# Kernel tuning notes

Hardware: AMD Instinct MI355X
Metric: run time of the kernel (lower is better)

Reference implementation:

```python
import jax, jax.numpy as jnp
import numpy as np

B, T, M, D, K, L = 128, 50, 4, 64, 64, 16  # batch, seq len, num_beh, embed dim, num_classes, capsule_length
NUM_ITEMS = 100000
R_ITERS = 3


def _dyn_gru(x, C, Wx, bx, Wh, bh):
    """Dynamic capsule GRU. x: [B,M,T,D], C: [B,M,T,K,L] (routing state modulates update gate).
    Returns final hidden beh_e [B,M,K,L] and per-step candidate states beh_N [B,M,T,K,L]."""
    # precompute input projections for all steps: [B,M,T,3,K,L]
    gi = (jnp.einsum('bmtd,mdg->bmtg', x, Wx) + bx[:, None, :]).reshape(x.shape[0], M, T, 3, K, L)

    def step(h, inp):
        gi_t, C_t = inp  # gi_t: [B,M,3,K,L], C_t: [B,M,K,L]
        gh = (jnp.einsum('bmkl,mklg->bmkg', h, Wh) + bh).reshape(h.shape[0], M, K, 3, L)
        r = jax.nn.sigmoid(gi_t[:, :, 0] + gh[:, :, :, 0])
        z = jax.nn.sigmoid(gi_t[:, :, 1] + gh[:, :, :, 1] + C_t)  # dynamic gate via routing state C
        n = jnp.tanh(gi_t[:, :, 2] + r * gh[:, :, :, 2])
        h_new = (1.0 - z) * n + z * h
        return h_new, n

    h0 = jnp.zeros((x.shape[0], M, K, L), x.dtype)
    h_fin, ns = jax.lax.scan(step, h0, (jnp.moveaxis(gi, 2, 0), jnp.moveaxis(C, 2, 0)))
    return h_fin, jnp.moveaxis(ns, 0, 2)


def setup_inputs() -> dict:
    key = jax.random.key(0)
    ks = jax.random.split(key, 9)
    names = ['purchase_seq', 'cart_seq', 'fav_seq', 'click_seq']
    seqs = {n: jax.random.randint(k, (B, T), 0, NUM_ITEMS + 1) for n, k in zip(names, ks[:4])}
    item_emb = jax.random.normal(ks[4], (NUM_ITEMS + 1, D), jnp.float32) * 0.02
    item_emb = item_emb.at[0].set(0.0)  # padding_idx=0
    W = 0.01 * jax.random.uniform(ks[5], (K, L, M, K), jnp.float32)
    W_coef = 0.1 * jax.random.normal(ks[6], (K, D + L, L), jnp.float32)
    alpha = jnp.ones((1,), jnp.float32) * K
    w = jnp.ones((K,), jnp.float32)
    bias = jnp.zeros((K,), jnp.float32)
    gru_Wx = 0.05 * jax.random.normal(ks[7], (M, D, 3 * K * L), jnp.float32)
    gru_bx = jnp.zeros((M, 3 * K * L), jnp.float32)
    gru_Wh = 0.05 * jax.random.normal(ks[8], (M, K, L, 3 * L), jnp.float32)
    gru_bh = jnp.zeros((M, K, 3 * L), jnp.float32)
    return dict(**seqs, item_emb=item_emb, W=W, W_coef=W_coef, alpha=alpha, w=w, bias=bias,
                gru_Wx=gru_Wx, gru_bx=gru_bx, gru_Wh=gru_Wh, gru_bh=gru_bh)


def reference(purchase_seq, cart_seq, fav_seq, click_seq, item_emb, W, W_coef,
              alpha, w, bias, gru_Wx, gru_bx, gru_Wh, gru_bh):
    sg = jax.lax.stop_gradient

    def embed(seq):
        mask = (seq != 0).astype(item_emb.dtype)[..., None]
        return item_emb[seq] * mask

    x = jnp.stack([embed(purchase_seq), embed(cart_seq), embed(fav_seq), embed(click_seq)], axis=1)  # [B,M,T,D]
    bsz = x.shape[0]
    b = jnp.zeros((bsz, K, K, 1), x.dtype)
    C = jnp.zeros((bsz, M, T, K, L), x.dtype)

    # routing iterations (all GRU outputs / W / alpha / w / bias / item_emb detached; W_coef live)
    for _ in range(R_ITERS - 1):
        beh_e, beh_N = _dyn_gru(sg(x), sg(C), sg(gru_Wx), sg(gru_bx), sg(gru_Wh), sg(gru_bh))
        beh_e = sg(beh_e).transpose(0, 2, 1, 3)  # [B,K,M,L]
        u = jnp.einsum('bctd,cdtC->bcCd', beh_e, sg(W))  # [B,K,K,L]
        c = jax.nn.softmax(b, axis=2)
        v = sg(alpha) * jnp.sum(c * u, axis=1)  # [B,K,L]
        v_ = jnp.linalg.norm(v, axis=-1) * sg(w) + sg(bias)  # [B,K]
        E = sg(item_emb)
        p = jax.nn.softmax(v_ @ E.T, axis=-1) @ E  # [B,D]
        p = jnp.broadcast_to(p[:, None, :], (bsz, K, D))
        r = jnp.einsum('bcd,cdD->bcD', jnp.concatenate([p, v], axis=-1), W_coef)  # [B,K,L]
        b = b + jnp.sum(u * r[:, None], axis=-1, keepdims=True)
        C = C + sg(beh_N) * r[:, None, None]

    beh_e, _ = _dyn_gru(x, C, gru_Wx, gru_bx, gru_Wh, gru_bh)
    beh_e = beh_e.transpose(0, 2, 1, 3)
    u_hat = jnp.einsum('bctd,cdtC->bcCd', beh_e, W)
    c = jax.nn.softmax(b, axis=2)
    v = alpha * jnp.sum(c * u_hat, axis=1)
    v_ = jnp.linalg.norm(v, axis=-1) * w + bias
    return v_ @ item_emb.T  # [B, num_items+1]
```

## Files before the change

### kernel.cpp

```cpp
#include <hip/hip_runtime.h>
#include <hip/hip_bf16.h>
#include <cstdint>
#include <cstddef>

#define B_   128
#define T_   50
#define M_   4
#define D_   64
#define K_   64
#define L_   16
#define NIT  100001
#define NBP3 256
#define CHUNK3 391
#define PSTRIDE 8320

typedef unsigned short u16;
typedef unsigned int   u32;
typedef __attribute__((ext_vector_type(8))) short short8;
typedef __attribute__((ext_vector_type(4))) short short4v;
typedef __attribute__((ext_vector_type(4))) float f32x4;

__device__ __forceinline__ float bf2f(u16 v){ u32 u = ((u32)v)<<16; float f; __builtin_memcpy(&f,&u,4); return f; }
__device__ __forceinline__ u16 f2bf(float f){
  u32 u; __builtin_memcpy(&u,&f,4);
  u32 r = (u + 0x7FFFu + ((u>>16)&1u)) >> 16;
  return (u16)r;
}
__device__ __forceinline__ float fexp(float x){ return __builtin_amdgcn_exp2f(x*1.4426950408889634f); }
__device__ __forceinline__ float fsig(float x){ return __builtin_amdgcn_rcpf(1.0f + fexp(-x)); }
__device__ __forceinline__ float ftanh(float x){ return 1.0f - 2.0f*__builtin_amdgcn_rcpf(1.0f + fexp(2.0f*x)); }
__device__ __forceinline__ void unpack8(const u32* s, short8& h, short8& l){
  #pragma unroll
  for (int q=0;q<8;q++){ h[q]=(short)(s[q]&0xFFFFu); l[q]=(short)(s[q]>>16); }
}

#define MFMA32(A,Bv,C) __builtin_amdgcn_mfma_f32_16x16x32_bf16(A,Bv,C,0,0,0)

#if __has_builtin(__builtin_amdgcn_mfma_f32_16x16x16bf16_1k)
__device__ __forceinline__ f32x4 mfma16(short4v a, short4v b, f32x4 c){
  return __builtin_amdgcn_mfma_f32_16x16x16bf16_1k(a,b,c,0,0,0);
}
#elif __has_builtin(__builtin_amdgcn_mfma_f32_16x16x16_bf16)
__device__ __forceinline__ f32x4 mfma16(short4v a, short4v b, f32x4 c){
  return __builtin_amdgcn_mfma_f32_16x16x16_bf16(a,b,c,0,0,0);
}
#else
__device__ __forceinline__ f32x4 mfma16(short4v a, short4v b, f32x4 c){
  asm("v_mfma_f32_16x16x16_bf16 %0, %1, %2, %0" : "+v"(c) : "v"(a), "v"(b));
  return c;
}
#endif

__global__ __launch_bounds__(256) void k_prep_x(const int* __restrict__ s0, const int* __restrict__ s1,
  const int* __restrict__ s2, const int* __restrict__ s3, const float* __restrict__ E,
  u16* __restrict__ xh, u16* __restrict__ xl)
{
  int id = blockIdx.x*256 + threadIdx.x;
  int e8 = id & 7;
  int rm = id >> 3;
  int m = rm / 6400; int r = rm - m*6400;
  int t = r >> 7, b = r & 127;
  const int* sq = (m==0)? s0 : (m==1)? s1 : (m==2)? s2 : s3;
  int idx = sq[b*T_ + t];
  float sc = (idx==0)? 0.0f : 1.0f;
  const float4* ep = (const float4*)(E + (size_t)idx*64 + e8*8);
  float4 v0 = ep[0], v1 = ep[1];
  float vals[8] = {v0.x,v0.y,v0.z,v0.w,v1.x,v1.y,v1.z,v1.w};
  u32 hw[4], lw[4];
  #pragma unroll
  for (int q=0;q<4;q++){
    float f0 = vals[2*q]*sc, f1 = vals[2*q+1]*sc;
    u16 h0 = f2bf(f0), h1 = f2bf(f1);
    u16 l0 = f2bf(f0 - bf2f(h0)), l1 = f2bf(f1 - bf2f(h1));
    hw[q] = (u32)h0 | ((u32)h1<<16);
    lw[q] = (u32)l0 | ((u32)l1<<16);
  }
  size_t off = (size_t)rm*64 + e8*8;
  uint4 hv; hv.x=hw[0]; hv.y=hw[1]; hv.z=hw[2]; hv.w=hw[3];
  uint4 lv; lv.x=lw[0]; lv.y=lw[1]; lv.z=lw[2]; lv.w=lw[3];
  *(uint4*)(xh + off) = hv;
  *(uint4*)(xl + off) = lv;
}

__global__ __launch_bounds__(256) void k_prep_w(const float* __restrict__ Wx,
  u16* __restrict__ wh, u16* __restrict__ wl)
{
  __shared__ float tl[64][65];
  int m = blockIdx.x / 48, gt = blockIdx.x % 48;
  for (int it=0; it<16; ++it){
    int li = threadIdx.x + it*256;
    int dl = li >> 6, gl = li & 63;
    tl[dl][gl] = Wx[((size_t)m*64 + dl)*3072 + gt*64 + gl];
  }
  __syncthreads();
  for (int it=0; it<2; ++it){
    int unit = threadIdx.x + it*256;
    int gl = unit >> 3, d8 = unit & 7;
    u32 hw[4], lw[4];
    #pragma unroll
    for (int q=0;q<4;q++){
      float f0 = tl[d8*8+2*q][gl], f1 = tl[d8*8+2*q+1][gl];
      u16 h0 = f2bf(f0), h1 = f2bf(f1);
      u16 l0 = f2bf(f0 - bf2f(h0)), l1 = f2bf(f1 - bf2f(h1));
      hw[q] = (u32)h0 | ((u32)h1<<16);
      lw[q] = (u32)l0 | ((u32)l1<<16);
    }
    size_t off = ((size_t)m*3072 + gt*64 + gl)*64 + d8*8;
    uint4 hv; hv.x=hw[0]; hv.y=hw[1]; hv.z=hw[2]; hv.w=hw[3];
    uint4 lv; lv.x=lw[0]; lv.y=lw[1]; lv.z=lw[2]; lv.w=lw[3];
    *(uint4*)(wh + off) = hv;
    *(uint4*)(wl + off) = lv;
  }
}

template<int PASS>
__global__ __launch_bounds__(256,2) void k_gru_mfma(
  const u16* __restrict__ xh, const u16* __restrict__ xl,
  const u16* __restrict__ wh, const u16* __restrict__ wl,
  const float* __restrict__ Wh, const float* __restrict__ bx, const float* __restrict__ bhp,
  const float* __restrict__ rp1, const float* __restrict__ rp2,
  const u16* __restrict__ Nr1, const u16* __restrict__ Nr2,
  u16* __restrict__ Nw, float* __restrict__ behE)
{
  int tid = threadIdx.x;
  int lane = tid & 63;
  int n16 = lane & 15, quad = lane >> 4;
  int j0 = quad*4;
  int wid = blockIdx.x*4 + (tid>>6);
  int bt = wid & 7, k = (wid>>3)&63, m = wid>>9;
  int b = bt*16 + n16;

  short8 WxH[3][2], WxL[3][2];
  #pragma unroll
  for (int g=0; g<3; ++g){
    int grow = g*1024 + k*16 + n16;
    #pragma unroll
    for (int c=0; c<2; ++c){
      size_t off = ((size_t)(m*3072 + grow))*64 + c*32 + quad*8;
      WxH[g][c] = *(const short8*)(wh + off);
      WxL[g][c] = *(const short8*)(wl + off);
    }
  }
  const float* whp = Wh + ((size_t)(m*64+k)*16)*48;
  short4v WhH[3], WhL[3];
  #pragma unroll
  for (int g=0; g<3; ++g){
    short4v hhv, llv;
    #pragma unroll
    for (int i=0;i<4;i++){
      float w = whp[(j0+i)*48 + g*16 + n16];
      u16 hbits = f2bf(w);
      hhv[i] = (short)hbits;
      llv[i] = (short)f2bf(w - bf2f(hbits));
    }
    WhH[g]=hhv; WhL[g]=llv;
  }
  float biasv[3][4], bhn[4];
  #pragma unroll
  for (int g=0; g<3; ++g)
    #pragma unroll
    for (int rg=0; rg<4; ++rg){
      int j = j0+rg;
      float tb = bx[m*3072 + g*1024 + k*16 + j];
      if (g<2) tb += bhp[(m*64+k)*48 + g*16 + j];
      biasv[g][rg] = tb;
    }
  #pragma unroll
  for (int rg=0; rg<4; ++rg) bhn[rg] = bhp[(m*64+k)*48 + 32 + j0 + rg];

  float rv1[4]={0.f,0.f,0.f,0.f}, rv2[4]={0.f,0.f,0.f,0.f};
  if (PASS>=2){
    float4 q = *(const float4*)(rp1 + ((size_t)b*64+k)*16 + j0);
    rv1[0]=q.x; rv1[1]=q.y; rv1[2]=q.z; rv1[3]=q.w;
  }
  if (PASS==3){
    float4 q = *(const float4*)(rp2 + ((size_t)b*64+k)*16 + j0);
    rv2[0]=q.x; rv2[1]=q.y; rv2[2]=q.z; rv2[3]=q.w;
  }

  size_t xrow  = ((size_t)m*6400 + bt*16 + n16)*64 + quad*8;
  size_t nbase = ((size_t)(m*64+k))*102400 + (size_t)b*16 + j0;

  short4v hH = {0,0,0,0}, hL = {0,0,0,0};
  float hprev[4] = {0.f,0.f,0.f,0.f};

  short8 cBh0 = *(const short8*)(xh + xrow);
  short8 cBh1 = *(const short8*)(xh + xrow + 32);
  short8 cBl0 = *(const short8*)(xl + xrow);
  short8 cBl1 = *(const short8*)(xl + xrow + 32);
  uint2 cN1 = {0,0}, cN2 = {0,0};
  if (PASS>=2) cN1 = *(const uint2*)(Nr1 + nbase);
  if (PASS==3) cN2 = *(const uint2*)(Nr2 + nbase);

  for (int t=0;t<50;++t){
    short8 nBh0, nBh1, nBl0, nBl1; uint2 nN1={0,0}, nN2={0,0};
    if (t<49){
      size_t xo = xrow + (size_t)(t+1)*8192;
      nBh0 = *(const short8*)(xh + xo);
      nBh1 = *(const short8*)(xh + xo + 32);
      nBl0 = *(const short8*)(xl + xo);
      nBl1 = *(const short8*)(xl + xo + 32);
      if (PASS>=2) nN1 = *(const uint2*)(Nr1 + nbase + (size_t)(t+1)*2048);
      if (PASS==3) nN2 = *(const uint2*)(Nr2 + nbase + (size_t)(t+1)*2048);
    }
    f32x4 giA[3];
    #pragma unroll
    for (int g=0; g<3; ++g){
      f32x4 a = {biasv[g][0], biasv[g][1], biasv[g][2], biasv[g][3]};
      a = MFMA32(WxH[g][0], cBh0, a);
      a = MFMA32(WxH[g][1], cBh1, a);
      a = MFMA32(WxL[g][0], cBh0, a);
      a = MFMA32(WxL[g][1], cBh1, a);
      a = MFMA32(WxH[g][0], cBl0, a);
      a = MFMA32(WxH[g][1], cBl1, a);
      giA[g] = a;
    }
    f32x4 ghr = {0.f,0.f,0.f,0.f};
    f32x4 ghz = {0.f,0.f,0.f,0.f};
    f32x4 ghn = {bhn[0], bhn[1], bhn[2], bhn[3]};
    ghr = mfma16(WhH[0], hH, ghr); ghr = mfma16(WhL[0], hH, ghr); ghr = mfma16(WhH[0], hL, ghr);
    ghz = mfma16(WhH[1], hH, ghz); ghz = mfma16(WhL[1], hH, ghz); ghz = mfma16(WhH[1], hL, ghz);
    ghn = mfma16(WhH[2], hH, ghn); ghn = mfma16(WhL[2], hH, ghn); ghn = mfma16(WhH[2], hL, ghn);

    u32 np0=0, np1=0;
    short4v hHn = {0,0,0,0}, hLn = {0,0,0,0};
    #pragma unroll
    for (int rg=0; rg<4; ++rg){
      float Ct = 0.f;
      if (PASS>=2){
        u32 wbits = (rg<2)? cN1.x : cN1.y;
        Ct = bf2f((u16)(wbits >> ((rg&1)*16))) * rv1[rg];
      }
      if (PASS==3){
        u32 wbits = (rg<2)? cN2.x : cN2.y;
        Ct += bf2f((u16)(wbits >> ((rg&1)*16))) * rv2[rg];
      }
      float rr = fsig(giA[0][rg] + ghr[rg]);
      float zz = fsig(giA[1][rg] + ghz[rg] + Ct);
      float nn = ftanh(giA[2][rg] + rr*ghn[rg]);
      float hv = nn + zz*(hprev[rg]-nn);
      hprev[rg] = hv;
      if (PASS<=2){
        u32 nb = f2bf(nn);
        if (rg==0) np0 |= nb;
        else if (rg==1) np0 |= nb<<16;
        else if (rg==2) np1 |= nb;
        else np1 |= nb<<16;
      }
      u16 hb = f2bf(hv);
      hHn[rg] = (short)hb;
      hLn[rg] = (short)f2bf(hv - bf2f(hb));
    }
    if (PASS<=2){
      uint2 st; st.x=np0; st.y=np1;
      *(uint2*)(Nw + nbase + (size_t)t*2048) = st;
    }
    hH = hHn; hL = hLn;
    if (t<49){
      cBh0=nBh0; cBh1=nBh1; cBl0=nBl0; cBl1=nBl1;
      cN1=nN1; cN2=nN2;
    }
  }
  float4 st; st.x=hprev[0]; st.y=hprev[1]; st.z=hprev[2]; st.w=hprev[3];
  *(float4*)(behE + (((size_t)b*64 + k)*4 + m)*16 + j0) = st;
}

__global__ __launch_bounds__(256) void k_cv(const float* __restrict__ bmat, const float* __restrict__ behE,
  const float* __restrict__ W, const float* __restrict__ alpha, const float* __restrict__ wv,
  const float* __restrict__ bias, float* __restrict__ vout, float* __restrict__ vT)
{
  __shared__ float cm[64][65];
  __shared__ float vsh[64][17];
  __shared__ float besh[4096];
  int b = blockIdx.x, tid = threadIdx.x;
  for (int it=0; it<16; ++it){
    int li = tid + it*256;
    cm[li>>6][li&63] = bmat[(size_t)b*4096 + li];
    besh[li] = behE[(size_t)b*4096 + li];
  }
  __syncthreads();
  if (tid < 64){
    float mx = -1e30f;
    for (int jj=0;jj<64;jj++) mx = fmaxf(mx, cm[tid][jj]);
    float sm = 0.f;
    for (int jj=0;jj<64;jj++){ float e = fexp(cm[tid][jj]-mx); cm[tid][jj]=e; sm+=e; }
    float inv = 1.0f/sm;
    for (int jj=0;jj<64;jj++) cm[tid][jj] *= inv;
  }
  __syncthreads();
  int j = tid & 63, dq = tid>>6;
  float a0=0,a1=0,a2=0,a3=0;
  for (int i=0;i<64;++i){
    float cij = cm[i][j];
    #pragma unroll
    for (int q=0;q<4;++q){
      int d = dq*4+q;
      const float* wp = W + ((size_t)((i*16+d)*4))*64 + j;
      float uu = besh[i*64+d]*wp[0] + besh[i*64+16+d]*wp[64]
               + besh[i*64+32+d]*wp[128] + besh[i*64+48+d]*wp[192];
      float cu = cij*uu;
      if (q==0) a0 += cu; else if (q==1) a1 += cu; else if (q==2) a2 += cu; else a3 += cu;
    }
  }
  float al = alpha[0];
  a0*=al; a1*=al; a2*=al; a3*=al;
  vsh[j][dq*4]=a0; vsh[j][dq*4+1]=a1; vsh[j][dq*4+2]=a2; vsh[j][dq*4+3]=a3;
  float* vp = vout + ((size_t)b*64 + j)*16 + dq*4;
  vp[0]=a0; vp[1]=a1; vp[2]=a2; vp[3]=a3;
  __syncthreads();
  if (tid < 64){
    float s=0.f;
    #pragma unroll
    for (int dd=0; dd<16; ++dd){ float q = vsh[tid][dd]; s += q*q; }
    vT[tid*128 + b] = sqrtf(s)*wv[tid] + bias[tid];
  }
}

__global__ __launch_bounds__(256) void k_prep_v(const float* __restrict__ vT, u32* __restrict__ vBp)
{
  int id = blockIdx.x*256 + threadIdx.x;
  int b = id>>6, c = id&63;
  float v = vT[c*128 + b];
  u16 h = f2bf(v); u16 l = f2bf(v - bf2f(h));
  vBp[id] = (u32)h | ((u32)l<<16);
}

__global__ __launch_bounds__(256) void k_pfused(const u32* __restrict__ vBp, const float* __restrict__ E,
  float* __restrict__ partial)
{
  __shared__ u16 etAh[32*72], etAl[32*72];
  __shared__ u16 etBh[64*32], etBl[64*32];
  __shared__ u32 exT[128*36];
  int tid = threadIdx.x, lane = tid&63, w = tid>>6;
  int n16 = lane&15, quad = lane>>4;

  short8 vh[2][2], vl[2][2];
  #pragma unroll
  for (int nt2=0; nt2<2; ++nt2){
    int b = (2*w+nt2)*16 + n16;
    #pragma unroll
    for (int s=0; s<2; ++s){
      u32 tmp[8];
      const u32* src = vBp + b*64 + s*32 + quad*8;
      #pragma unroll
      for (int q=0;q<8;q++) tmp[q]=src[q];
      unpack8(tmp, vh[nt2][s], vl[nt2][s]);
    }
  }
  f32x4 pacc[2][4];
  #pragma unroll
  for (int a2=0;a2<2;a2++)
    #pragma unroll
    for (int b2=0;b2<4;b2++){ pacc[a2][b2][0]=0.f; pacc[a2][b2][1]=0.f; pacc[a2][b2][2]=0.f; pacc[a2][b2][3]=0.f; }
  float srun[2] = {0.f, 0.f};

  int start = blockIdx.x*CHUNK3;
  int bend = start + CHUNK3; if (bend > NIT) bend = NIT;
  int sitem = tid>>3, sc0 = (tid&7)*8;
  for (int ch=0; ch<13; ++ch){
    int i0 = start + ch*32;
    if (i0 >= bend) break;
    {
      int gidx = i0 + sitem;
      float vals[8];
      if (gidx < NIT){
        float4 a = ((const float4*)E)[(size_t)gidx*16 + (sc0>>2)];
        float4 b2 = ((const float4*)E)[(size_t)gidx*16 + (sc0>>2) + 1];
        vals[0]=a.x; vals[1]=a.y; vals[2]=a.z; vals[3]=a.w;
        vals[4]=b2.x; vals[5]=b2.y; vals[6]=b2.z; vals[7]=b2.w;
      } else {
        #pragma unroll
        for (int q=0;q<8;q++) vals[q]=0.f;
      }
      u16 hh[8], ll[8];
      #pragma unroll
      for (int q=0;q<8;q++){ hh[q]=f2bf(vals[q]); ll[q]=f2bf(vals[q]-bf2f(hh[q])); }
      *(short8*)(etAh + sitem*72 + sc0) = *(short8*)hh;
      *(short8*)(etAl + sitem*72 + sc0) = *(short8*)ll;
      #pragma unroll
      for (int q=0;q<8;q++){
        etBh[(sc0+q)*32 + sitem] = hh[q];
        etBl[(sc0+q)*32 + sitem] = ll[q];
      }
    }
    __syncthreads();
    short8 Eh[2][2], El[2][2];
    #pragma unroll
    for (int mt=0; mt<2; ++mt)
      #pragma unroll
      for (int s=0; s<2; ++s){
        const u16* base = etAh + (mt*16 + n16)*72 + s*32 + quad*8;
        Eh[mt][s] = *(const short8*)base;
        El[mt][s] = *(const short8*)(etAl + (mt*16 + n16)*72 + s*32 + quad*8);
      }
    #pragma unroll
    for (int mt=0; mt<2; ++mt){
      #pragma unroll
      for (int nt2=0; nt2<2; ++nt2){
        f32x4 a = {0.f,0.f,0.f,0.f};
        #pragma unroll
        for (int s=0; s<2; ++s){
          a = __builtin_amdgcn_mfma_f32_16x16x32_bf16(Eh[mt][s], vh[nt2][s], a, 0,0,0);
          a = __builtin_amdgcn_mfma_f32_16x16x32_bf16(Eh[mt][s], vl[nt2][s], a, 0,0,0);
          a = __builtin_amdgcn_mfma_f32_16x16x32_bf16(El[mt][s], vh[nt2][s], a, 0,0,0);
        }
        u32 packed[4];
        #pragma unroll
        for (int rg=0; rg<4; ++rg){
          int it_g = i0 + mt*16 + quad*4 + rg;
          float ex = (it_g < bend)? fexp(a[rg]) : 0.f;
          srun[nt2] += ex;
          u16 h = f2bf(ex); u16 l = f2bf(ex - bf2f(h));
          packed[rg] = (u32)h | ((u32)l<<16);
        }
        int bl = (2*w+nt2)*16 + n16;
        uint4 st; st.x=packed[0]; st.y=packed[1]; st.z=packed[2]; st.w=packed[3];
        *(uint4*)(exT + bl*36 + mt*16 + quad*4) = st;
      }
    }
    __syncthreads();
    short8 Xh[2], Xl[2];
    #pragma unroll
    for (int mt2=0; mt2<2; ++mt2){
      int bl = (2*w+mt2)*16 + n16;
      uint4 t0 = *(const uint4*)(exT + bl*36 + quad*8);
      uint4 t1 = *(const uint4*)(exT + bl*36 + quad*8 + 4);
      u32 tmp[8] = {t0.x,t0.y,t0.z,t0.w,t1.x,t1.y,t1.z,t1.w};
      unpack8(tmp, Xh[mt2], Xl[mt2]);
    }
    #pragma unroll
    for (int nt3=0; nt3<4; ++nt3){
      int d = nt3*16 + n16;
      short8 Bh = *(const short8*)(etBh + d*32 + quad*8);
      short8 Bl = *(const short8*)(etBl + d*32 + quad*8);
      #pragma unroll
      for (int mt2=0; mt2<2; ++mt2){
        pacc[mt2][nt3] = __builtin_amdgcn_mfma_f32_16x16x32_bf16(Xh[mt2], Bh, pacc[mt2][nt3], 0,0,0);
        pacc[mt2][nt3] = __builtin_amdgcn_mfma_f32_16x16x32_bf16(Xh[mt2], Bl, pacc[mt2][nt3], 0,0,0);
        pacc[mt2][nt3] = __builtin_amdgcn_mfma_f32_16x16x32_bf16(Xl[mt2], Bh, pacc[mt2][nt3], 0,0,0);
      }
    }
    __syncthreads();
  }
  float* dst = partial + (size_t)blockIdx.x*PSTRIDE;
  #pragma unroll
  for (int mt2=0; mt2<2; ++mt2)
    #pragma unroll
    for (int nt3=0; nt3<4; ++nt3)
      #pragma unroll
      for (int rg=0; rg<4; ++rg){
        int b_g = (2*w+mt2)*16 + quad*4 + rg;
        int d_g = nt3*16 + n16;
        dst[b_g*64 + d_g] = pacc[mt2][nt3][rg];
      }
  #pragma unroll
  for (int nt2=0; nt2<2; ++nt2){
    float vsum = srun[nt2];
    vsum += __shfl_xor(vsum, 16);
    vsum += __shfl_xor(vsum, 32);
    if (quad == 0) dst[8192 + (2*w+nt2)*16 + n16] = vsum;
  }
}

__global__ __launch_bounds__(256) void k_pcomb(const float* __restrict__ partial, float* __restrict__ p)
{
  int id = blockIdx.x*256 + threadIdx.x;
  int b = id>>6;
  float a = 0.f, s = 0.f;
  for (int q=0;q<NBP3;q++){
    a += partial[(size_t)q*PSTRIDE + id];
    s += partial[(size_t)q*PSTRIDE + 8192 + b];
  }
  p[id] = a/s;
}

__global__ __launch_bounds__(256) void k_r(const float* __restrict__ p, const float* __restrict__ v,
  const float* __restrict__ Wc, float* __restrict__ r, float* __restrict__ rT)
{
  int gid = blockIdx.x*256 + threadIdx.x;
  int l = gid & 15, j = (gid>>4)&63, b = gid>>10;
  const float* wc = Wc + ((size_t)j*80)*16 + l;
  const float* pbp = p + b*64;
  float acc = 0.f;
  #pragma unroll 8
  for (int d=0; d<64; ++d) acc += pbp[d]*wc[d*16];
  const float* vb = v + ((size_t)b*64 + j)*16;
  #pragma unroll
  for (int d=0; d<16; ++d) acc += vb[d]*wc[(64+d)*16];
  r[((size_t)b*64+j)*16 + l] = acc;
  rT[((size_t)b*16+l)*64 + j] = acc;
}

__global__ __launch_bounds__(256) void k_bupd(const float* __restrict__ behE, const float* __restrict__ W,
  const float* __restrict__ rT, float* __restrict__ bmat)
{
  int lane = threadIdx.x & 63;
  int idx = blockIdx.x*4 + (threadIdx.x>>6);
  int b = idx >> 6, i = idx & 63;
  const float* be = behE + (size_t)idx*64;
  const float* rp = rT + (size_t)b*1024;
  float acc = 0.f;
  #pragma unroll
  for (int d=0; d<16; ++d){
    const float* wp = W + ((size_t)((i*16+d)*4))*64 + lane;
    float uu = be[d]*wp[0] + be[16+d]*wp[64] + be[32+d]*wp[128] + be[48+d]*wp[192];
    acc += uu * rp[d*64 + lane];
  }
  bmat[(size_t)idx*64 + lane] += acc;
}

__global__ __launch_bounds__(256) void k_logits(const u32* __restrict__ vBp, const float* __restrict__ E,
  float* __restrict__ out)
{
  __shared__ u16 etAh[64*72], etAl[64*72];
  __shared__ float lt[128*68];
  int tid = threadIdx.x, lane = tid&63, w = tid>>6;
  int n16 = lane&15, quad = lane>>4;
  short8 vh[2][2], vl[2][2];
  #pragma unroll
  for (int nt2=0; nt2<2; ++nt2){
    int b = (2*w+nt2)*16 + n16;
    #pragma unroll
    for (int s=0; s<2; ++s){
      u32 tmp[8];
      const u32* src = vBp + b*64 + s*32 + quad*8;
      #pragma unroll
      for (int q=0;q<8;q++) tmp[q]=src[q];
      unpack8(tmp, vh[nt2][s], vl[nt2][s]);
    }
  }
  int i0 = blockIdx.x*64;
  {
    int sitem = tid>>2, sc0 = (tid&3)*16;
    int gidx = i0 + sitem;
    float vals[16];
    if (gidx < NIT){
      #pragma unroll
      for (int q=0;q<4;q++){
        float4 a = ((const float4*)E)[(size_t)gidx*16 + (sc0>>2) + q];
        vals[4*q]=a.x; vals[4*q+1]=a.y; vals[4*q+2]=a.z; vals[4*q+3]=a.w;
      }
    } else {
      #pragma unroll
      for (int q=0;q<16;q++) vals[q]=0.f;
    }
    u16 hh[16], ll[16];
    #pragma unroll
    for (int q=0;q<16;q++){ hh[q]=f2bf(vals[q]); ll[q]=f2bf(vals[q]-bf2f(hh[q])); }
    *(short8*)(etAh + sitem*72 + sc0)     = *(short8*)hh;
    *(short8*)(etAh + sitem*72 + sc0 + 8) = *(short8*)(hh+8);
    *(short8*)(etAl + sitem*72 + sc0)     = *(short8*)ll;
    *(short8*)(etAl + sitem*72 + sc0 + 8) = *(short8*)(ll+8);
  }
  __syncthreads();
  #pragma unroll
  for (int mt=0; mt<4; ++mt){
    short8 Eh[2], El[2];
    #pragma unroll
    for (int s=0; s<2; ++s){
      Eh[s] = *(const short8*)(etAh + (mt*16 + n16)*72 + s*32 + quad*8);
      El[s] = *(const short8*)(etAl + (mt*16 + n16)*72 + s*32 + quad*8);
    }
    #pragma unroll
    for (int nt2=0; nt2<2; ++nt2){
      f32x4 a = {0.f,0.f,0.f,0.f};
      #pragma unroll
      for (int s=0; s<2; ++s){
        a = __builtin_amdgcn_mfma_f32_16x16x32_bf16(Eh[s], vh[nt2][s], a, 0,0,0);
        a = __builtin_amdgcn_mfma_f32_16x16x32_bf16(Eh[s], vl[nt2][s], a, 0,0,0);
        a = __builtin_amdgcn_mfma_f32_16x16x32_bf16(El[s], vh[nt2][s], a, 0,0,0);
      }
      int b = (2*w+nt2)*16 + n16;
      *(float4*)(lt + b*68 + mt*16 + quad*4) = *(float4*)&a;
    }
  }
  __syncthreads();
  int col = tid & 63, rgp = tid >> 6;
  if (i0 + col < NIT){
    #pragma unroll
    for (int rr=0; rr<32; ++rr){
      int b = rgp*32 + rr;
      out[(size_t)b*NIT + i0 + col] = lt[b*68 + col];
    }
  }
}

extern "C" void kernel_launch(void* const* d_in, const int* in_sizes, int n_in,
                              void* d_out, int out_size, void* d_ws, size_t ws_size,
                              hipStream_t stream)
{
  (void)in_sizes; (void)n_in; (void)out_size; (void)ws_size;
  const int*   s0 = (const int*)d_in[0];
  const int*   s1 = (const int*)d_in[1];
  const int*   s2 = (const int*)d_in[2];
  const int*   s3 = (const int*)d_in[3];
  const float* E  = (const float*)d_in[4];
  const float* W  = (const float*)d_in[5];
  const float* Wc = (const float*)d_in[6];
  const float* alpha = (const float*)d_in[7];
  const float* wv    = (const float*)d_in[8];
  const float* bias  = (const float*)d_in[9];
  const float* Wx = (const float*)d_in[10];
  const float* bx = (const float*)d_in[11];
  const float* Wh = (const float*)d_in[12];
  const float* bh = (const float*)d_in[13];

  char* ws = (char*)d_ws;
  size_t off = 0;
  auto alloc = [&](size_t bytes)->void*{ void* q = ws + off; off += (bytes + 255) & ~(size_t)255; return q; };
  u16*   N1   = (u16*)  alloc((size_t)M_*K_*T_*B_*16*2);
  u16*   N2   = (u16*)  alloc((size_t)M_*K_*T_*B_*16*2);
  u16*   xh   = (u16*)  alloc((size_t)M_*6400*64*2);
  u16*   xl   = (u16*)  alloc((size_t)M_*6400*64*2);
  u16*   wh   = (u16*)  alloc((size_t)M_*3072*64*2);
  u16*   wl   = (u16*)  alloc((size_t)M_*3072*64*2);
  float* bmat = (float*)alloc((size_t)B_*64*64*4);
  float* behE = (float*)alloc((size_t)B_*64*4*16*4);
  float* v    = (float*)alloc((size_t)B_*64*16*4);
  float* vT   = (float*)alloc((size_t)64*128*4);
  u32*   vBp  = (u32*)  alloc((size_t)128*64*4);
  float* r1   = (float*)alloc((size_t)B_*64*16*4);
  float* rT1  = (float*)alloc((size_t)B_*64*16*4);
  float* r2   = (float*)alloc((size_t)B_*64*16*4);
  float* rT2  = (float*)alloc((size_t)B_*64*16*4);
  float* p    = (float*)alloc((size_t)B_*64*4);
  float* partial = (float*)alloc((size_t)NBP3*PSTRIDE*4);

  hipMemsetAsync(bmat, 0, (size_t)B_*64*64*4, stream);
  k_prep_x<<<800,256,0,stream>>>(s0,s1,s2,s3,E,xh,xl);
  k_prep_w<<<192,256,0,stream>>>(Wx,wh,wl);

  k_gru_mfma<1><<<512,256,0,stream>>>(xh,xl,wh,wl,Wh,bx,bh,
                                      nullptr,nullptr,nullptr,nullptr, N1, behE);
  k_cv<<<128,256,0,stream>>>(bmat,behE,W,alpha,wv,bias,v,vT);
  k_prep_v<<<32,256,0,stream>>>(vT,vBp);
  k_pfused<<<NBP3,256,0,stream>>>(vBp,E,partial);
  k_pcomb<<<32,256,0,stream>>>(partial,p);
  k_r<<<512,256,0,stream>>>(p,v,Wc,r1,rT1);
  k_bupd<<<2048,256,0,stream>>>(behE,W,rT1,bmat);

  k_gru_mfma<2><<<512,256,0,stream>>>(xh,xl,wh,wl,Wh,bx,bh,
                                      r1,nullptr, N1,nullptr, N2, behE);
  k_cv<<<128,256,0,stream>>>(bmat,behE,W,alpha,wv,bias,v,vT);
  k_prep_v<<<32,256,0,stream>>>(vT,vBp);
  k_pfused<<<NBP3,256,0,stream>>>(vBp,E,partial);
  k_pcomb<<<32,256,0,stream>>>(partial,p);
  k_r<<<512,256,0,stream>>>(p,v,Wc,r2,rT2);
  k_bupd<<<2048,256,0,stream>>>(behE,W,rT2,bmat);

  k_gru_mfma<3><<<512,256,0,stream>>>(xh,xl,wh,wl,Wh,bx,bh,
                                      r1,r2, N1,N2, nullptr, behE);
  k_cv<<<128,256,0,stream>>>(bmat,behE,W,alpha,wv,bias,v,vT);
  k_prep_v<<<32,256,0,stream>>>(vT,vBp);
  k_logits<<<1563,256,0,stream>>>(vBp,E,(float*)d_out);
}
```

Before: 513.5 us.

## Process two capsule classes per wave in GRU kernel to share x loads

```diff
diff --git a/kernel.cpp b/kernel.cpp
--- a/kernel.cpp
+++ b/kernel.cpp
@@ -114,7 +114,7 @@
 }
 
 template<int PASS>
-__global__ __launch_bounds__(256,2) void k_gru_mfma(
+__global__ __launch_bounds__(256,1) void k_gru_mfma(
   const u16* __restrict__ xh, const u16* __restrict__ xl,
   const u16* __restrict__ wh, const u16* __restrict__ wl,
   const float* __restrict__ Wh, const float* __restrict__ bx, const float* __restrict__ bhp,
@@ -127,142 +127,151 @@
   int n16 = lane & 15, quad = lane >> 4;
   int j0 = quad*4;
   int wid = blockIdx.x*4 + (tid>>6);
-  int bt = wid & 7, k = (wid>>3)&63, m = wid>>9;
+  int bt = wid & 7, k0 = (wid>>3)&31, m = wid>>8;
   int b = bt*16 + n16;
 
-  short8 WxH[3][2], WxL[3][2];
-  #pragma unroll
-  for (int g=0; g<3; ++g){
-    int grow = g*1024 + k*16 + n16;
-    #pragma unroll
-    for (int c=0; c<2; ++c){
-      size_t off = ((size_t)(m*3072 + grow))*64 + c*32 + quad*8;
-      WxH[g][c] = *(const short8*)(wh + off);
-      WxL[g][c] = *(const short8*)(wl + off);
-    }
-  }
-  const float* whp = Wh + ((size_t)(m*64+k)*16)*48;
-  short4v WhH[3], WhL[3];
-  #pragma unroll
-  for (int g=0; g<3; ++g){
-    short4v hhv, llv;
-    #pragma unroll
-    for (int i=0;i<4;i++){
-      float w = whp[(j0+i)*48 + g*16 + n16];
-      u16 hbits = f2bf(w);
-      hhv[i] = (short)hbits;
-      llv[i] = (short)f2bf(w - bf2f(hbits));
-    }
-    WhH[g]=hhv; WhL[g]=llv;
-  }
-  float biasv[3][4], bhn[4];
-  #pragma unroll
-  for (int g=0; g<3; ++g)
-    #pragma unroll
-    for (int rg=0; rg<4; ++rg){
-      int j = j0+rg;
-      float tb = bx[m*3072 + g*1024 + k*16 + j];
-      if (g<2) tb += bhp[(m*64+k)*48 + g*16 + j];
-      biasv[g][rg] = tb;
-    }
-  #pragma unroll
-  for (int rg=0; rg<4; ++rg) bhn[rg] = bhp[(m*64+k)*48 + 32 + j0 + rg];
-
-  float rv1[4]={0.f,0.f,0.f,0.f}, rv2[4]={0.f,0.f,0.f,0.f};
-  if (PASS>=2){
-    float4 q = *(const float4*)(rp1 + ((size_t)b*64+k)*16 + j0);
-    rv1[0]=q.x; rv1[1]=q.y; rv1[2]=q.z; rv1[3]=q.w;
-  }
-  if (PASS==3){
-    float4 q = *(const float4*)(rp2 + ((size_t)b*64+k)*16 + j0);
-    rv2[0]=q.x; rv2[1]=q.y; rv2[2]=q.z; rv2[3]=q.w;
-  }
-
-  size_t xrow  = ((size_t)m*6400 + bt*16 + n16)*64 + quad*8;
-  size_t nbase = ((size_t)(m*64+k))*102400 + (size_t)b*16 + j0;
-
-  short4v hH = {0,0,0,0}, hL = {0,0,0,0};
-  float hprev[4] = {0.f,0.f,0.f,0.f};
-
-  short8 cBh0 = *(const short8*)(xh + xrow);
-  short8 cBh1 = *(const short8*)(xh + xrow + 32);
-  short8 cBl0 = *(const short8*)(xl + xrow);
-  short8 cBl1 = *(const short8*)(xl + xrow + 32);
-  uint2 cN1 = {0,0}, cN2 = {0,0};
-  if (PASS>=2) cN1 = *(const uint2*)(Nr1 + nbase);
-  if (PASS==3) cN2 = *(const uint2*)(Nr2 + nbase);
-
-  for (int t=0;t<50;++t){
-    short8 nBh0, nBh1, nBl0, nBl1; uint2 nN1={0,0}, nN2={0,0};
-    if (t<49){
-      size_t xo = xrow + (size_t)(t+1)*8192;
-      nBh0 = *(const short8*)(xh + xo);
-      nBh1 = *(const short8*)(xh + xo + 32);
-      nBl0 = *(const short8*)(xl + xo);
-      nBl1 = *(const short8*)(xl + xo + 32);
-      if (PASS>=2) nN1 = *(const uint2*)(Nr1 + nbase + (size_t)(t+1)*2048);
-      if (PASS==3) nN2 = *(const uint2*)(Nr2 + nbase + (size_t)(t+1)*2048);
-    }
-    f32x4 giA[3];
+  short8 WxH[2][3][2], WxL[2][3][2];
+  short4v WhH[2][3], WhL[2][3];
+  float biasv[2][3][4], bhn[2][4];
+  float rv1[2][4], rv2[2][4];
+  size_t nbase[2];
+
+  #pragma unroll
+  for (int c=0;c<2;++c){
+    int k = k0 + 32*c;
     #pragma unroll
     for (int g=0; g<3; ++g){
-      f32x4 a = {biasv[g][0], biasv[g][1], biasv[g][2], biasv[g][3]};
-      a = MFMA32(WxH[g][0], cBh0, a);
-      a = MFMA32(WxH[g][1], cBh1, a);
-      a = MFMA32(WxL[g][0], cBh0, a);
-      a = MFMA32(WxL[g][1], cBh1, a);
-      a = MFMA32(WxH[g][0], cBl0, a);
-      a = MFMA32(WxH[g][1], cBl1, a);
-      giA[g] = a;
-    }
-    f32x4 ghr = {0.f,0.f,0.f,0.f};
-    f32x4 ghz = {0.f,0.f,0.f,0.f};
-    f32x4 ghn = {bhn[0], bhn[1], bhn[2], bhn[3]};
-    ghr = mfma16(WhH[0], hH, ghr); ghr = mfma16(WhL[0], hH, ghr); ghr = mfma16(WhH[0], hL, ghr);
-    ghz = mfma16(WhH[1], hH, ghz); ghz = mfma16(WhL[1], hH, ghz); ghz = mfma16(WhH[1], hL, ghz);
-    ghn = mfma16(WhH[2], hH, ghn); ghn = mfma16(WhL[2], hH, ghn); ghn = mfma16(WhH[2], hL, ghn);
-
-    u32 np0=0, np1=0;
-    short4v hHn = {0,0,0,0}, hLn = {0,0,0,0};
-    #pragma unroll
-    for (int rg=0; rg<4; ++rg){
-      float Ct = 0.f;
-      if (PASS>=2){
-        u32 wbits = (rg<2)? cN1.x : cN1.y;
-        Ct = bf2f((u16)(wbits >> ((rg&1)*16))) * rv1[rg];
-      }
-      if (PASS==3){
-        u32 wbits = (rg<2)? cN2.x : cN2.y;
-        Ct += bf2f((u16)(wbits >> ((rg&1)*16))) * rv2[rg];
-      }
-      float rr = fsig(giA[0][rg] + ghr[rg]);
-      float zz = fsig(giA[1][rg] + ghz[rg] + Ct);
-      float nn = ftanh(giA[2][rg] + rr*ghn[rg]);
-      float hv = nn + zz*(hprev[rg]-nn);
-      hprev[rg] = hv;
-      if (PASS<=2){
-        u32 nb = f2bf(nn);
-        if (rg==0) np0 |= nb;
-        else if (rg==1) np0 |= nb<<16;
-        else if (rg==2) np1 |= nb;
-        else np1 |= nb<<16;
-      }
-      u16 hb = f2bf(hv);
-      hHn[rg] = (short)hb;
-      hLn[rg] = (short)f2bf(hv - bf2f(hb));
-    }
-    if (PASS<=2){
-      uint2 st; st.x=np0; st.y=np1;
-      *(uint2*)(Nw + nbase + (size_t)t*2048) = st;
-    }
-    hH = hHn; hL = hLn;
-    if (t<49){
-      cBh0=nBh0; cBh1=nBh1; cBl0=nBl0; cBl1=nBl1;
-      cN1=nN1; cN2=nN2;
-    }
-  }
-  float4 st; st.x=hprev[0]; st.y=hprev[1]; st.z=hprev[2]; st.w=hprev[3];
-  *(float4*)(behE + (((size_t)b*64 + k)*4 + m)*16 + j0) = st;
+      int grow = g*1024 + k*16 + n16;
+      #pragma unroll
+      for (int h2=0; h2<2; ++h2){
+        size_t off = ((size_t)(m*3072 + grow))*64 + h2*32 + quad*8;
+        WxH[c][g][h2] = *(const short8*)(wh + off);
+        WxL[c][g][h2] = *(const short8*)(wl + off);
+      }
+    }
+    const float* whp = Wh + ((size_t)(m*64+k)*16)*48;
+    #pragma unroll
+    for (int g=0; g<3; ++g){
+      short4v hhv, llv;
+      #pragma unroll
+      for (int i=0;i<4;i++){
+        float w = whp[(j0+i)*48 + g*16 + n16];
+        u16 hbits = f2bf(w);
+        hhv[i] = (short)hbits;
+        llv[i] = (short)f2bf(w - bf2f(hbits));
+      }
+      WhH[c][g]=hhv; WhL[c][g]=llv;
+    }
+    #pragma unroll
+    for (int g=0; g<3; ++g)
+      #pragma unroll
+      for (int rg=0; rg<4; ++rg){
+        int j = j0+rg;
+        float tb = bx[m*3072 + g*1024 + k*16 + j];
+        if (g<2) tb += bhp[(m*64+k)*48 + g*16 + j];
+        biasv[c][g][rg] = tb;
+      }
+    #pragma unroll
+    for (int rg=0; rg<4; ++rg) bhn[c][rg] = bhp[(m*64+k)*48 + 32 + j0 + rg];
+    if (PASS>=2){
+      float4 q = *(const float4*)(rp1 + ((size_t)b*64+k)*16 + j0);
+      rv1[c][0]=q.x; rv1[c][1]=q.y; rv1[c][2]=q.z; rv1[c][3]=q.w;
+    } else { rv1[c][0]=rv1[c][1]=rv1[c][2]=rv1[c][3]=0.f; }
+    if (PASS==3){
+      float4 q = *(const float4*)(rp2 + ((size_t)b*64+k)*16 + j0);
+      rv2[c][0]=q.x; rv2[c][1]=q.y; rv2[c][2]=q.z; rv2[c][3]=q.w;
+    } else { rv2[c][0]=rv2[c][1]=rv2[c][2]=rv2[c][3]=0.f; }
+    nbase[c] = ((size_t)(m*64+k))*102400 + (size_t)b*16 + j0;
+  }
+
+  size_t xrow = ((size_t)m*6400 + bt*16 + n16)*64 + quad*8;
+
+  short4v hH[2] = {{0,0,0,0},{0,0,0,0}}, hL[2] = {{0,0,0,0},{0,0,0,0}};
+  float hprev[2][4] = {{0.f,0.f,0.f,0.f},{0.f,0.f,0.f,0.f}};
+
+  short8 cB0 = *(const short8*)(xh + xrow);
+  short8 cB1 = *(const short8*)(xh + xrow + 32);
+  short8 cB2 = *(const short8*)(xl + xrow);
+  short8 cB3 = *(const short8*)(xl + xrow + 32);
+  uint2 cN1[2]={{0,0},{0,0}}, cN2[2]={{0,0},{0,0}};
+  if (PASS>=2){ cN1[0] = *(const uint2*)(Nr1 + nbase[0]); cN1[1] = *(const uint2*)(Nr1 + nbase[1]); }
+  if (PASS==3){ cN2[0] = *(const uint2*)(Nr2 + nbase[0]); cN2[1] = *(const uint2*)(Nr2 + nbase[1]); }
+
+#define GRU_STEP(tt) { \
+  _Pragma("unroll") \
+  for (int c=0;c<2;++c){ \
+    f32x4 giA[3]; \
+    _Pragma("unroll") \
+    for (int g=0; g<3; ++g){ \
+      f32x4 a = {biasv[c][g][0], biasv[c][g][1], biasv[c][g][2], biasv[c][g][3]}; \
+      a = MFMA32(WxH[c][g][0], cB0, a); \
+      a = MFMA32(WxH[c][g][1], cB1, a); \
+      a = MFMA32(WxL[c][g][0], cB0, a); \
+      a = MFMA32(WxL[c][g][1], cB1, a); \
+      a = MFMA32(WxH[c][g][0], cB2, a); \
+      a = MFMA32(WxH[c][g][1], cB3, a); \
+      giA[g] = a; \
+    } \
+    f32x4 ghr = {0.f,0.f,0.f,0.f}; \
+    f32x4 ghz = {0.f,0.f,0.f,0.f}; \
+    f32x4 ghn = {bhn[c][0], bhn[c][1], bhn[c][2], bhn[c][3]}; \
+    ghr = mfma16(WhH[c][0], hH[c], ghr); ghr = mfma16(WhL[c][0], hH[c], ghr); ghr = mfma16(WhH[c][0], hL[c], ghr); \
+    ghz = mfma16(WhH[c][1], hH[c], ghz); ghz = mfma16(WhL[c][1], hH[c], ghz); ghz = mfma16(WhH[c][1], hL[c], ghz); \
+    ghn = mfma16(WhH[c][2], hH[c], ghn); ghn = mfma16(WhL[c][2], hH[c], ghn); ghn = mfma16(WhH[c][2], hL[c], ghn); \
+    u32 np0=0, np1=0; \
+    short4v hHn = {0,0,0,0}, hLn = {0,0,0,0}; \
+    _Pragma("unroll") \
+    for (int rg=0; rg<4; ++rg){ \
+      float Ct = 0.f; \
+      if (PASS>=2){ u32 wb = (rg<2)? cN1[c].x : cN1[c].y; Ct = bf2f((u16)(wb >> ((rg&1)*16))) * rv1[c][rg]; } \
+      if (PASS==3){ u32 wb = (rg<2)? cN2[c].x : cN2[c].y; Ct += bf2f((u16)(wb >> ((rg&1)*16))) * rv2[c][rg]; } \
+      float rr = fsig(giA[0][rg] + ghr[rg]); \
+      float zz = fsig(giA[1][rg] + ghz[rg] + Ct); \
+      float nn = ftanh(giA[2][rg] + rr*ghn[rg]); \
+      float hv = nn + zz*(hprev[c][rg]-nn); \
+      hprev[c][rg] = hv; \
+      if (PASS<=2){ \
+        u32 nb = f2bf(nn); \
+        if (rg==0) np0 |= nb; else if (rg==1) np0 |= nb<<16; else if (rg==2) np1 |= nb; else np1 |= nb<<16; \
+      } \
+      u16 hb = f2bf(hv); \
+      hHn[rg] = (short)hb; \
+      hLn[rg] = (short)f2bf(hv - bf2f(hb)); \
+    } \
+    if (PASS<=2){ uint2 stv; stv.x=np0; stv.y=np1; *(uint2*)(Nw + nbase[c] + (size_t)(tt)*2048) = stv; } \
+    hH[c] = hHn; hL[c] = hLn; \
+  } \
+}
+
+  for (int t=0;t<49;++t){
+    size_t xo = xrow + (size_t)(t+1)*8192;
+    short8 nB0 = *(const short8*)(xh + xo);
+    short8 nB1 = *(const short8*)(xh + xo + 32);
+    short8 nB2 = *(const short8*)(xl + xo);
+    short8 nB3 = *(const short8*)(xl + xo + 32);
+    uint2 nN1[2]={{0,0},{0,0}}, nN2[2]={{0,0},{0,0}};
+    if (PASS>=2){
+      nN1[0] = *(const uint2*)(Nr1 + nbase[0] + (size_t)(t+1)*2048);
+      nN1[1] = *(const uint2*)(Nr1 + nbase[1] + (size_t)(t+1)*2048);
+    }
+    if (PASS==3){
+      nN2[0] = *(const uint2*)(Nr2 + nbase[0] + (size_t)(t+1)*2048);
+      nN2[1] = *(const uint2*)(Nr2 + nbase[1] + (size_t)(t+1)*2048);
+    }
+    GRU_STEP(t);
+    cB0=nB0; cB1=nB1; cB2=nB2; cB3=nB3;
+    if (PASS>=2){ cN1[0]=nN1[0]; cN1[1]=nN1[1]; }
+    if (PASS==3){ cN2[0]=nN2[0]; cN2[1]=nN2[1]; }
+  }
+  GRU_STEP(49);
+#undef GRU_STEP
+
+  #pragma unroll
+  for (int c=0;c<2;++c){
+    int k = k0 + 32*c;
+    float4 stv; stv.x=hprev[c][0]; stv.y=hprev[c][1]; stv.z=hprev[c][2]; stv.w=hprev[c][3];
+    *(float4*)(behE + (((size_t)b*64 + k)*4 + m)*16 + j0) = stv;
+  }
 }
 
 __global__ __launch_bounds__(256) void k_cv(const float* __restrict__ bmat, const float* __restrict__ behE,
@@ -389,8 +398,7 @@
     for (int mt=0; mt<2; ++mt)
       #pragma unroll
       for (int s=0; s<2; ++s){
-        const u16* base = etAh + (mt*16 + n16)*72 + s*32 + quad*8;
-        Eh[mt][s] = *(const short8*)base;
+        Eh[mt][s] = *(const short8*)(etAh + (mt*16 + n16)*72 + s*32 + quad*8);
         El[mt][s] = *(const short8*)(etAl + (mt*16 + n16)*72 + s*32 + quad*8);
       }
     #pragma unroll
@@ -630,7 +638,7 @@
   k_prep_x<<<800,256,0,stream>>>(s0,s1,s2,s3,E,xh,xl);
   k_prep_w<<<192,256,0,stream>>>(Wx,wh,wl);
 
-  k_gru_mfma<1><<<512,256,0,stream>>>(xh,xl,wh,wl,Wh,bx,bh,
+  k_gru_mfma<1><<<256,256,0,stream>>>(xh,xl,wh,wl,Wh,bx,bh,
                                       nullptr,nullptr,nullptr,nullptr, N1, behE);
   k_cv<<<128,256,0,stream>>>(bmat,behE,W,alpha,wv,bias,v,vT);
   k_prep_v<<<32,256,0,stream>>>(vT,vBp);
@@ -639,7 +647,7 @@
   k_r<<<512,256,0,stream>>>(p,v,Wc,r1,rT1);
   k_bupd<<<2048,256,0,stream>>>(behE,W,rT1,bmat);
 
-  k_gru_mfma<2><<<512,256,0,stream>>>(xh,xl,wh,wl,Wh,bx,bh,
+  k_gru_mfma<2><<<256,256,0,stream>>>(xh,xl,wh,wl,Wh,bx,bh,
                                       r1,nullptr, N1,nullptr, N2, behE);
   k_cv<<<128,256,0,stream>>>(bmat,behE,W,alpha,wv,bias,v,vT);
   k_prep_v<<<32,256,0,stream>>>(vT,vBp);
@@ -648,7 +656,7 @@
   k_r<<<512,256,0,stream>>>(p,v,Wc,r2,rT2);
   k_bupd<<<2048,256,0,stream>>>(behE,W,rT2,bmat);
 
-  k_gru_mfma<3><<<512,256,0,stream>>>(xh,xl,wh,wl,Wh,bx,bh,
+  k_gru_mfma<3><<<256,256,0,stream>>>(xh,xl,wh,wl,Wh,bx,bh,
                                       r1,r2, N1,N2, nullptr, behE);
   k_cv<<<128,256,0,stream>>>(bmat,behE,W,alpha,wv,bias,v,vT);
   k_prep_v<<<32,256,0,stream>>>(vT,vBp);
```

Result: faster. 500.0 us (-2.6%).
